# Kernel optimization log

Measured on AMD Instinct MI355X. Metric: run time of the kernel, lower is better.

The kernel has to match this reference:

```python
import jax, jax.numpy as jnp
import numpy as np

N = 4096
INPUT_DIM = 512
KEY_DIM = 64
OUT_DIM = 512
N_HEADS = 8


def _xavier_normal(key, shape, gain):
    # torch xavier_normal_ on [heads, fan_in, fan_out]: fan over last two dims
    fan_in, fan_out = shape[-2], shape[-1]
    std = gain * (2.0 / (fan_in + fan_out)) ** 0.5
    return jax.random.normal(key, shape, dtype=jnp.float32) * std


def setup_inputs() -> dict:
    key = jax.random.key(0)
    kx, ka, kk, kq, kv, ko = jax.random.split(key, 6)
    gain = 2.0 ** 0.5
    node_matrix = jax.random.normal(kx, (N, INPUT_DIM), dtype=jnp.float32)
    adjacency_matrix = jax.random.randint(ka, (N, N), 0, 2).astype(jnp.float32)
    Wks = _xavier_normal(kk, (N_HEADS, INPUT_DIM, KEY_DIM), gain)
    Wqs = _xavier_normal(kq, (N_HEADS, INPUT_DIM, KEY_DIM), gain)
    Wvs = _xavier_normal(kv, (N_HEADS, INPUT_DIM, KEY_DIM), gain)
    Wo = _xavier_normal(ko, (N_HEADS, KEY_DIM, OUT_DIM), gain)
    return {"node_matrix": node_matrix, "adjacency_matrix": adjacency_matrix,
            "Wks": Wks, "Wqs": Wqs, "Wvs": Wvs, "Wo": Wo}


def reference(node_matrix, adjacency_matrix, Wks, Wqs, Wvs, Wo):
    n = adjacency_matrix.shape[0]
    # force self-loops
    adj = jnp.maximum(adjacency_matrix, jnp.eye(n, dtype=adjacency_matrix.dtype))
    # per-head projections: [heads, N, key_dim]
    keys = jnp.einsum('nj,hjk->hnk', node_matrix, Wks)
    queries = jnp.einsum('nj,hjk->hnk', node_matrix, Wqs)
    values = jnp.einsum('nj,hjk->hnk', node_matrix, Wvs)
    key_dim = Wks.shape[-1]
    # [heads, N(query), N(key)] scores, scaled and adjacency-masked
    atts = jnp.einsum('hqk,hmk->hqm', queries, keys) / (key_dim ** 0.5)
    atts = atts - 1e16 * (1.0 - adj)[None, :, :]
    atts = jax.nn.softmax(atts, axis=-1)
    # weighted values, then output projection, summed over heads -> [N, out_dim]
    return jnp.einsum('hqm,hmk,hko->qo', atts, values, Wo)
```

## Files before the change

### kernel.cpp

```cpp
#include <hip/hip_runtime.h>
#include <stdint.h>

typedef unsigned short u16;
typedef __attribute__((ext_vector_type(8))) __bf16 bf16x8;
typedef __attribute__((ext_vector_type(8))) short short8;
typedef __attribute__((ext_vector_type(4))) float f32x4;

#define N_NODES 4096
#define DMODEL  512
#define QKVLD   1536
#define KD      64
#define NH      8
#define NSPLIT  2
#define LOG2E   1.4426950408889634f

static __device__ __forceinline__ u16 f2bf(float f) {
  unsigned u = __builtin_bit_cast(unsigned, f);
  u += 0x7fffu + ((u >> 16) & 1u);
  return (u16)(u >> 16);
}

static __device__ __forceinline__ f32x4 mfma16(short8 a, short8 b, f32x4 c) {
  return __builtin_amdgcn_mfma_f32_16x16x32_bf16(
      __builtin_bit_cast(bf16x8, a), __builtin_bit_cast(bf16x8, b), c, 0, 0, 0);
}

static __device__ __forceinline__ void gload16(const u16* g, u16* l) {
  __builtin_amdgcn_global_load_lds((const __attribute__((address_space(1))) void*)g,
                                   (__attribute__((address_space(3))) void*)l, 16, 0, 0);
}


__global__ void conv_bf16(const float* __restrict__ in, u16* __restrict__ out, int n4) {
  int i = blockIdx.x * blockDim.x + threadIdx.x;
  if (i < n4) {
    float4 v = ((const float4*)in)[i];
    ushort4 o; o.x = f2bf(v.x); o.y = f2bf(v.y); o.z = f2bf(v.z); o.w = f2bf(v.w);
    ((ushort4*)out)[i] = o;
  }
}

__global__ void pack_qkv(const float* __restrict__ Wq, const float* __restrict__ Wk,
                         const float* __restrict__ Wv, u16* __restrict__ Wt) {
  __shared__ float t[64][65];
  int z = blockIdx.z;
  int mat = z >> 3, h = z & 7;
  const float* src = (mat == 0) ? Wq : ((mat == 1) ? Wk : Wv);
  float scale = (mat == 0) ? 0.125f * LOG2E : 1.0f;
  src += (size_t)h * DMODEL * KD;
  u16* dst = Wt + ((size_t)mat * DMODEL + (size_t)h * KD) * DMODEL;
  int r0 = blockIdx.x * 64;
  int tid = threadIdx.x, lc = tid & 63;
#pragma unroll
  for (int i = 0; i < 16; ++i) {
    int row = i * 4 + (tid >> 6);
    t[row][lc] = src[(size_t)(r0 + row) * KD + lc];
  }
  __syncthreads();
#pragma unroll
  for (int i = 0; i < 16; ++i) {
    int row = i * 4 + (tid >> 6);
    dst[(size_t)row * DMODEL + r0 + lc] = f2bf(t[lc][row] * scale);
  }
}

__global__ void pack_wo(const float* __restrict__ Wo, u16* __restrict__ Wot) {
  __shared__ float t[64][65];
  int r0 = blockIdx.x * 64, c0 = blockIdx.y * 64;
  int tid = threadIdx.x, lc = tid & 63;
#pragma unroll
  for (int i = 0; i < 16; ++i) {
    int row = i * 4 + (tid >> 6);
    t[row][lc] = Wo[(size_t)(r0 + row) * 512 + c0 + lc];
  }
  __syncthreads();
#pragma unroll
  for (int i = 0; i < 16; ++i) {
    int row = i * 4 + (tid >> 6);
    Wot[(size_t)(c0 + row) * 512 + r0 + lc] = f2bf(t[lc][row]);
  }
}

__global__ void build_bits(const float* __restrict__ adj, unsigned long long* __restrict__ bits) {
  int gw = (blockIdx.x * blockDim.x + threadIdx.x) >> 6;
  int lane = threadIdx.x & 63;
  int nw = (gridDim.x * blockDim.x) >> 6;
  for (int word = gw; word < N_NODES * 64; word += nw) {
    int q = word >> 6, wc = word & 63;
    int k = wc * 64 + lane;
    float v = adj[(size_t)q * N_NODES + k];
    unsigned long long m = __ballot((v != 0.0f) || (q == k));
    if (lane == 0) bits[word] = m;
  }
}

template <bool OUT_BF16>
__global__ __launch_bounds__(256) void gemm_nt(const u16* __restrict__ A,
                                               const u16* __restrict__ Bt,
                                               void* __restrict__ C, int K,
                                               int lda, int ldb, int ldc,
                                               u16* __restrict__ Vt) {
  __shared__ __align__(16) u16 lA[64 * 64];
  __shared__ __align__(16) u16 lB[64 * 64];
  const int m0 = blockIdx.x * 64, n0 = blockIdx.y * 64;
  const int tid = threadIdx.x;
  const int w = tid >> 6, lane = tid & 63, lm = lane & 15, lg = lane >> 4;
  const int srow = tid >> 2, sc0 = tid & 3;
  f32x4 acc[4] = {};
  for (int k0 = 0; k0 < K; k0 += 64) {
    __syncthreads();
    {
      const short8* ga = (const short8*)(A + (size_t)(m0 + srow) * lda + k0);
      short8* la = (short8*)(lA + srow * 64);
      la[sc0 ^ (srow & 7)] = ga[sc0];
      la[(sc0 + 4) ^ (srow & 7)] = ga[sc0 + 4];
      const short8* gb = (const short8*)(Bt + (size_t)(n0 + srow) * ldb + k0);
      short8* lb = (short8*)(lB + srow * 64);
      lb[sc0 ^ (srow & 7)] = gb[sc0];
      lb[(sc0 + 4) ^ (srow & 7)] = gb[sc0 + 4];
    }
    __syncthreads();
    short8 af0, af1;
    {
      int row = w * 16 + lm;
      af0 = ((short8*)(lA + row * 64))[lg ^ (row & 7)];
      af1 = ((short8*)(lA + row * 64))[(4 + lg) ^ (row & 7)];
    }
#pragma unroll
    for (int nt = 0; nt < 4; ++nt) {
      int row = nt * 16 + lm;
      short8 b0 = ((short8*)(lB + row * 64))[lg ^ (row & 7)];
      short8 b1 = ((short8*)(lB + row * 64))[(4 + lg) ^ (row & 7)];
      acc[nt] = mfma16(af0, b0, acc[nt]);
      acc[nt] = mfma16(af1, b1, acc[nt]);
    }
  }
#pragma unroll
  for (int nt = 0; nt < 4; ++nt) {
    int n = n0 + nt * 16 + lm;
    int mb = m0 + w * 16 + lg * 4;
    if (OUT_BF16) {
      ushort4 o4;
#pragma unroll
      for (int r = 0; r < 4; ++r) ((u16*)&o4)[r] = f2bf(acc[nt][r]);
#pragma unroll
      for (int r = 0; r < 4; ++r) ((u16*)C)[(size_t)(mb + r) * ldc + n] = ((u16*)&o4)[r];
      if (Vt != nullptr && n >= 1024)
        *(ushort4*)(Vt + (size_t)(n - 1024) * N_NODES + mb) = o4;
    } else {
#pragma unroll
      for (int r = 0; r < 4; ++r)
        ((float*)C)[(size_t)(mb + r) * ldc + n] = acc[nt][r];
    }
  }
}

__global__ __launch_bounds__(256, 2) void attn_kernel(const u16* __restrict__ QKV,
                                                      const u16* __restrict__ Vt,
                                                      const unsigned long long* __restrict__ bits,
                                                      float* __restrict__ Op,
                                                      float* __restrict__ lp) {
  __shared__ __align__(16) u16 LDSA[16384 + 4 * 2304];
  const int bid = blockIdx.x;
  const int h = bid & 7, sp = (bid >> 3) & 1, qb = bid >> 4;
  const int tid = threadIdx.x;
  const int w = tid >> 6, lane = tid & 63, lm = lane & 15, lg = lane >> 4;
  const int lg4 = lg * 4;
  const int kb0 = sp * 32;

  const int q0 = qb * 128 + w * 32 + lm;
  const int q1 = q0 + 16;

  const short8 qf00 = *(const short8*)(QKV + (size_t)q0 * QKVLD + h * 64 + lg * 8);
  const short8 qf01 = *(const short8*)(QKV + (size_t)q0 * QKVLD + h * 64 + 32 + lg * 8);
  const short8 qf10 = *(const short8*)(QKV + (size_t)q1 * QKVLD + h * 64 + lg * 8);
  const short8 qf11 = *(const short8*)(QKV + (size_t)q1 * QKVLD + h * 64 + 32 + lg * 8);

  short8 ones;
#pragma unroll
  for (int j = 0; j < 8; ++j) ones[j] = (short)0x3F80;

  const int a0 = lm * 64 + (lg ^ (lm & 7)) * 8;
  const u16* rdA = LDSA + a0;
  const u16* rdB = LDSA + (a0 ^ 32);
  u16* pW0 = LDSA + 16384 + w * 2304 + lm * 72 + lg4;
  u16* pW1 = pW0 + 1152;
  const u16* pR0 = LDSA + 16384 + w * 2304 + lm * 72 + lg * 8;
  const u16* pR1 = pR0 + 1152;

  const int srow = lane >> 3, sc = lane & 7;
  const u16* kP[2]; const u16* vP[2];
#pragma unroll
  for (int i = 0; i < 2; ++i) {
    int row = w * 16 + i * 8 + srow;
    kP[i] = QKV + (size_t)(kb0 * 64 + row) * QKVLD + 512 + h * 64 + (sc ^ (row & 7)) * 8;
    vP[i] = Vt + ((size_t)h * 64 + row) * N_NODES + kb0 * 64 + (sc ^ (row & 7)) * 8;
  }

#define STAGE(buf) do {                                               \
    gload16(kP[0], LDSA + (buf) * 4096 + (w * 2 + 0) * 512);          \
    gload16(kP[1], LDSA + (buf) * 4096 + (w * 2 + 1) * 512);          \
    gload16(vP[0], LDSA + 8192 + (buf) * 4096 + (w * 2 + 0) * 512);   \
    gload16(vP[1], LDSA + 8192 + (buf) * 4096 + (w * 2 + 1) * 512);   \
  } while (0)
#define ADV() do { kP[0] += 64 * QKVLD; kP[1] += 64 * QKVLD; vP[0] += 64; vP[1] += 64; } while (0)

  f32x4 of0[4] = {}, of1[4] = {};
  f32x4 la0 = {}, la1 = {};
  const unsigned long long* bp0 = bits + (size_t)q0 * 64 + kb0;
  const unsigned long long* bp1 = bits + (size_t)q1 * 64 + kb0;

  STAGE(0);
  unsigned long long wb0 = bp0[0], wb1 = bp1[0];

#define SMPACK(sv, wbv, pW, pR, la, paA, paB)                                  \
  do {                                                                         \
    unsigned wlo = (unsigned)((wbv) >> lg4);                                   \
    unsigned whi = ((unsigned)((wbv) >> 32)) >> lg4;                           \
    _Pragma("unroll")                                                          \
    for (int kt = 0; kt < 4; ++kt) {                                           \
      unsigned word = (kt < 2) ? wlo : whi;                                    \
      float pv[4];                                                             \
      _Pragma("unroll")                                                        \
      for (int r = 0; r < 4; ++r) {                                            \
        float e = __builtin_amdgcn_exp2f(sv[kt][r]);                           \
        int mb;                                                                \
        asm("v_bfe_i32 %0, %1, %2, 1" : "=v"(mb)                               \
            : "v"(word), "n"((kt & 1) * 16 + r));                              \
        pv[r] = __builtin_bit_cast(float,                                      \
                   __builtin_bit_cast(unsigned, e) & (unsigned)mb);            \
      }                                                                        \
      unsigned pk0, pk1;                                                       \
      asm("v_cvt_pk_bf16_f32 %0, %1, %2" : "=v"(pk0) : "v"(pv[0]), "v"(pv[1]));\
      asm("v_cvt_pk_bf16_f32 %0, %1, %2" : "=v"(pk1) : "v"(pv[2]), "v"(pv[3]));\
      uint2 pr; pr.x = pk0; pr.y = pk1;                                        \
      *(uint2*)(pW + kt * 16) = pr;                                            \
    }                                                                          \
    paA = *(const short8*)(pR);                                                \
    paB = *(const short8*)(pR + 32);                                           \
    la = mfma16(ones, paA, la);                                                \
    la = mfma16(ones, paB, la);                                                \
  } while (0)

#define BODY(buf, i)                                                           \
  do {                                                                         \
    asm volatile("s_waitcnt vmcnt(0)" ::: "memory");                           \
    __builtin_amdgcn_s_barrier();                                              \
    if ((i) + 1 < 32) { ADV(); STAGE(buf ^ 1); }                               \
    unsigned long long nb0 = ((i) + 1 < 32) ? bp0[(i) + 1] : 0ull;             \
    unsigned long long nb1 = ((i) + 1 < 32) ? bp1[(i) + 1] : 0ull;             \
    f32x4 s0[4], s1[4];                                                        \
    _Pragma("unroll")                                                          \
    for (int kt = 0; kt < 4; ++kt) {                                           \
      short8 k0 = *(const short8*)(rdA + (buf) * 4096 + kt * 1024);            \
      short8 k1 = *(const short8*)(rdB + (buf) * 4096 + kt * 1024);            \
      f32x4 z0 = {0.f, 0.f, 0.f, 0.f}, z1 = {0.f, 0.f, 0.f, 0.f};              \
      z0 = mfma16(k0, qf00, z0); s0[kt] = mfma16(k1, qf01, z0);                \
      z1 = mfma16(k0, qf10, z1); s1[kt] = mfma16(k1, qf11, z1);                \
    }                                                                          \
    short8 pa00, pa01, pa10, pa11;                                             \
    SMPACK(s0, wb0, pW0, pR0, la0, pa00, pa01);                                \
    SMPACK(s1, wb1, pW1, pR1, la1, pa10, pa11);                                \
    _Pragma("unroll")                                                          \
    for (int dt = 0; dt < 4; ++dt) {                                           \
      short8 v0 = *(const short8*)(rdA + 8192 + (buf) * 4096 + dt * 1024);     \
      short8 v1 = *(const short8*)(rdB + 8192 + (buf) * 4096 + dt * 1024);     \
      of0[dt] = mfma16(v0, pa00, of0[dt]);                                     \
      of0[dt] = mfma16(v1, pa01, of0[dt]);                                     \
      of1[dt] = mfma16(v0, pa10, of1[dt]);                                     \
      of1[dt] = mfma16(v1, pa11, of1[dt]);                                     \
    }                                                                          \
    wb0 = nb0; wb1 = nb1;                                                      \
  } while (0)

#pragma unroll 1
  for (int it = 0; it < 16; ++it) {
    BODY(0, it * 2);
    BODY(1, it * 2 + 1);
  }
#undef BODY
#undef SMPACK
#undef STAGE
#undef ADV

  float* Ob = Op + (size_t)sp * N_NODES * DMODEL;
#pragma unroll
  for (int dt = 0; dt < 4; ++dt) {
    *(f32x4*)(Ob + (size_t)q0 * DMODEL + h * 64 + dt * 16 + lg4) = of0[dt];
    *(f32x4*)(Ob + (size_t)q1 * DMODEL + h * 64 + dt * 16 + lg4) = of1[dt];
  }
  if (lg == 0) {
    lp[((size_t)sp * NH + h) * N_NODES + q0] = la0[0];
    lp[((size_t)sp * NH + h) * N_NODES + q1] = la1[0];
  }
}

__global__ __launch_bounds__(256) void combine_kernel(const float* __restrict__ Op,
                                                      const float* __restrict__ lp,
                                                      u16* __restrict__ Oc) {
  int i = blockIdx.x * 256 + threadIdx.x;
  int col = (i * 4) & (DMODEL - 1);
  int q = (i * 4) >> 9;
  int h = col >> 6;
  float4 a = ((const float4*)Op)[i];
  float4 b = ((const float4*)(Op + (size_t)N_NODES * DMODEL))[i];
  float l = lp[(size_t)h * N_NODES + q] + lp[((size_t)NH + h) * N_NODES + q];
  float inv = 1.0f / l;
  ushort4 o;
  o.x = f2bf((a.x + b.x) * inv);
  o.y = f2bf((a.y + b.y) * inv);
  o.z = f2bf((a.z + b.z) * inv);
  o.w = f2bf((a.w + b.w) * inv);
  ((ushort4*)Oc)[i] = o;
}


extern "C" void kernel_launch(void* const* d_in, const int* in_sizes, int n_in,
                              void* d_out, int out_size, void* d_ws, size_t ws_size,
                              hipStream_t stream) {
  const float* X   = (const float*)d_in[0];
  const float* Adj = (const float*)d_in[1];
  const float* Wks = (const float*)d_in[2];
  const float* Wqs = (const float*)d_in[3];
  const float* Wvs = (const float*)d_in[4];
  const float* Wo  = (const float*)d_in[5];

  char* p = (char*)d_ws;
  u16* Xb  = (u16*)p; p += (size_t)N_NODES * DMODEL * 2;
  u16* Wt  = (u16*)p; p += (size_t)3 * DMODEL * DMODEL * 2;
  u16* Wot = (u16*)p; p += (size_t)DMODEL * DMODEL * 2;
  u16* QKV = (u16*)p; p += (size_t)N_NODES * QKVLD * 2;
  u16* Vt  = (u16*)p; p += (size_t)N_NODES * DMODEL * 2;
  u16* Oc  = (u16*)p; p += (size_t)N_NODES * DMODEL * 2;
  unsigned long long* bits = (unsigned long long*)p; p += (size_t)N_NODES * 64 * 8;
  float* Op = (float*)p; p += (size_t)NSPLIT * N_NODES * DMODEL * 4;
  float* lp = (float*)p; p += (size_t)NSPLIT * NH * N_NODES * 4;

  conv_bf16<<<dim3(2048), dim3(256), 0, stream>>>(X, Xb, N_NODES * DMODEL / 4);
  pack_qkv<<<dim3(8, 1, 24), dim3(256), 0, stream>>>(Wqs, Wks, Wvs, Wt);
  pack_wo<<<dim3(8, 8), dim3(256), 0, stream>>>(Wo, Wot);
  build_bits<<<dim3(2048), dim3(256), 0, stream>>>(Adj, bits);

  gemm_nt<true><<<dim3(64, 24), dim3(256), 0, stream>>>(Xb, Wt, QKV, 512, 512, 512, QKVLD, Vt);

  attn_kernel<<<dim3(512), dim3(256), 0, stream>>>(QKV, Vt, bits, Op, lp);
  combine_kernel<<<dim3(N_NODES * DMODEL / 4 / 256), dim3(256), 0, stream>>>(Op, lp, Oc);

  gemm_nt<false><<<dim3(64, 8), dim3(256), 0, stream>>>(Oc, Wot, d_out, 512, 512, 512, 512, nullptr);
}
```

Before: 114.6 us.

## Software-pipeline attention loop across QK, softmax and PV stages

Restructures the attention main loop into a three-stage software pipeline. Each iteration computes QK scores for block i, the masked exp/pack softmax for block i-1 and the PV accumulation for block i-2, with a prologue and epilogue to fill and drain the pipeline. The goal is to let MFMA work from different stages overlap the exp and LDS round-trip latency that previously serialized within each block. To support this, V staging uses four LDS buffers and the per-wave P scratch is shrunk to a single shared region. The cost is more live registers (two sets of score and P fragments), which risks spills under the two-blocks-per-CU launch bound, plus a larger LDS footprint.

```diff
diff --git a/kernel.cpp b/kernel.cpp
--- a/kernel.cpp
+++ b/kernel.cpp
@@ -160,7 +160,7 @@
                                                       const unsigned long long* __restrict__ bits,
                                                       float* __restrict__ Op,
                                                       float* __restrict__ lp) {
-  __shared__ __align__(16) u16 LDSA[16384 + 4 * 2304];
+  __shared__ __align__(16) u16 LDSA[24576 + 4 * 1152];
   const int bid = blockIdx.x;
   const int h = bid & 7, sp = (bid >> 3) & 1, qb = bid >> 4;
   const int tid = threadIdx.x;
@@ -183,10 +183,8 @@
   const int a0 = lm * 64 + (lg ^ (lm & 7)) * 8;
   const u16* rdA = LDSA + a0;
   const u16* rdB = LDSA + (a0 ^ 32);
-  u16* pW0 = LDSA + 16384 + w * 2304 + lm * 72 + lg4;
-  u16* pW1 = pW0 + 1152;
-  const u16* pR0 = LDSA + 16384 + w * 2304 + lm * 72 + lg * 8;
-  const u16* pR1 = pR0 + 1152;
+  u16* pWx = LDSA + 24576 + w * 1152 + lm * 72 + lg4;
+  const u16* pRx = LDSA + 24576 + w * 1152 + lm * 72 + lg * 8;
 
   const int srow = lane >> 3, sc = lane & 7;
   const u16* kP[2]; const u16* vP[2];
@@ -197,11 +195,11 @@
     vP[i] = Vt + ((size_t)h * 64 + row) * N_NODES + kb0 * 64 + (sc ^ (row & 7)) * 8;
   }
 
-#define STAGE(buf) do {                                               \
-    gload16(kP[0], LDSA + (buf) * 4096 + (w * 2 + 0) * 512);          \
-    gload16(kP[1], LDSA + (buf) * 4096 + (w * 2 + 1) * 512);          \
-    gload16(vP[0], LDSA + 8192 + (buf) * 4096 + (w * 2 + 0) * 512);   \
-    gload16(vP[1], LDSA + 8192 + (buf) * 4096 + (w * 2 + 1) * 512);   \
+#define STAGE(kbuf, vbuf) do {                                          \
+    gload16(kP[0], LDSA + (kbuf) * 4096 + (w * 2 + 0) * 512);           \
+    gload16(kP[1], LDSA + (kbuf) * 4096 + (w * 2 + 1) * 512);           \
+    gload16(vP[0], LDSA + 8192 + (vbuf) * 4096 + (w * 2 + 0) * 512);    \
+    gload16(vP[1], LDSA + 8192 + (vbuf) * 4096 + (w * 2 + 1) * 512);    \
   } while (0)
 #define ADV() do { kP[0] += 64 * QKVLD; kP[1] += 64 * QKVLD; vP[0] += 64; vP[1] += 64; } while (0)
 
@@ -210,10 +208,23 @@
   const unsigned long long* bp0 = bits + (size_t)q0 * 64 + kb0;
   const unsigned long long* bp1 = bits + (size_t)q1 * 64 + kb0;
 
-  STAGE(0);
-  unsigned long long wb0 = bp0[0], wb1 = bp1[0];
-
-#define SMPACK(sv, wbv, pW, pR, la, paA, paB)                                  \
+  f32x4 sA0[4], sA1[4], sB0[4], sB1[4];
+  short8 paA00, paA01, paA10, paA11, paB00, paB01, paB10, paB11;
+  unsigned long long wb0, wb1;
+
+#define QKPH(kbuf, S0, S1)                                                     \
+  do {                                                                         \
+    _Pragma("unroll")                                                          \
+    for (int kt = 0; kt < 4; ++kt) {                                           \
+      short8 k0 = *(const short8*)(rdA + (kbuf) * 4096 + kt * 1024);           \
+      short8 k1 = *(const short8*)(rdB + (kbuf) * 4096 + kt * 1024);           \
+      f32x4 z0 = {0.f, 0.f, 0.f, 0.f}, z1 = {0.f, 0.f, 0.f, 0.f};              \
+      z0 = mfma16(k0, qf00, z0); S0[kt] = mfma16(k1, qf01, z0);                \
+      z1 = mfma16(k0, qf10, z1); S1[kt] = mfma16(k1, qf11, z1);                \
+    }                                                                          \
+  } while (0)
+
+#define SMPK(sv, wbv, la, paA, paB)                                            \
   do {                                                                         \
     unsigned wlo = (unsigned)((wbv) >> lg4);                                   \
     unsigned whi = ((unsigned)((wbv) >> 32)) >> lg4;                           \
@@ -234,52 +245,77 @@
       asm("v_cvt_pk_bf16_f32 %0, %1, %2" : "=v"(pk0) : "v"(pv[0]), "v"(pv[1]));\
       asm("v_cvt_pk_bf16_f32 %0, %1, %2" : "=v"(pk1) : "v"(pv[2]), "v"(pv[3]));\
       uint2 pr; pr.x = pk0; pr.y = pk1;                                        \
-      *(uint2*)(pW + kt * 16) = pr;                                            \
+      *(uint2*)(pWx + kt * 16) = pr;                                           \
     }                                                                          \
-    paA = *(const short8*)(pR);                                                \
-    paB = *(const short8*)(pR + 32);                                           \
+    paA = *(const short8*)(pRx);                                               \
+    paB = *(const short8*)(pRx + 32);                                          \
     la = mfma16(ones, paA, la);                                                \
     la = mfma16(ones, paB, la);                                                \
   } while (0)
 
-#define BODY(buf, i)                                                           \
+#define PVPH(vbuf, p00, p01, p10, p11)                                         \
+  do {                                                                         \
+    _Pragma("unroll")                                                          \
+    for (int dt = 0; dt < 4; ++dt) {                                           \
+      short8 v0 = *(const short8*)(rdA + 8192 + (vbuf) * 4096 + dt * 1024);    \
+      short8 v1 = *(const short8*)(rdB + 8192 + (vbuf) * 4096 + dt * 1024);    \
+      of0[dt] = mfma16(v0, p00, of0[dt]);                                      \
+      of0[dt] = mfma16(v1, p01, of0[dt]);                                      \
+      of1[dt] = mfma16(v0, p10, of1[dt]);                                      \
+      of1[dt] = mfma16(v1, p11, of1[dt]);                                      \
+    }                                                                          \
+  } while (0)
+
+#define ITERM(IDX, KBQ, SQ0, SQ1, DO_STAGE, KST, VST, DO_SM, SS0, SS1,         \
+              PW00, PW01, PW10, PW11, DO_PV, VPV, PR00, PR01, PR10, PR11)      \
   do {                                                                         \
     asm volatile("s_waitcnt vmcnt(0)" ::: "memory");                           \
     __builtin_amdgcn_s_barrier();                                              \
-    if ((i) + 1 < 32) { ADV(); STAGE(buf ^ 1); }                               \
-    unsigned long long nb0 = ((i) + 1 < 32) ? bp0[(i) + 1] : 0ull;             \
-    unsigned long long nb1 = ((i) + 1 < 32) ? bp1[(i) + 1] : 0ull;             \
-    f32x4 s0[4], s1[4];                                                        \
-    _Pragma("unroll")                                                          \
-    for (int kt = 0; kt < 4; ++kt) {                                           \
-      short8 k0 = *(const short8*)(rdA + (buf) * 4096 + kt * 1024);            \
-      short8 k1 = *(const short8*)(rdB + (buf) * 4096 + kt * 1024);            \
-      f32x4 z0 = {0.f, 0.f, 0.f, 0.f}, z1 = {0.f, 0.f, 0.f, 0.f};              \
-      z0 = mfma16(k0, qf00, z0); s0[kt] = mfma16(k1, qf01, z0);                \
-      z1 = mfma16(k0, qf10, z1); s1[kt] = mfma16(k1, qf11, z1);                \
+    if (DO_STAGE) { ADV(); STAGE(KST, VST); }                                  \
+    unsigned long long nb0 = bp0[IDX], nb1 = bp1[IDX];                         \
+    QKPH(KBQ, SQ0, SQ1);                                                       \
+    if (DO_SM) {                                                               \
+      SMPK(SS0, wb0, la0, PW00, PW01);                                         \
+      SMPK(SS1, wb1, la1, PW10, PW11);                                         \
     }                                                                          \
-    short8 pa00, pa01, pa10, pa11;                                             \
-    SMPACK(s0, wb0, pW0, pR0, la0, pa00, pa01);                                \
-    SMPACK(s1, wb1, pW1, pR1, la1, pa10, pa11);                                \
-    _Pragma("unroll")                                                          \
-    for (int dt = 0; dt < 4; ++dt) {                                           \
-      short8 v0 = *(const short8*)(rdA + 8192 + (buf) * 4096 + dt * 1024);     \
-      short8 v1 = *(const short8*)(rdB + 8192 + (buf) * 4096 + dt * 1024);     \
-      of0[dt] = mfma16(v0, pa00, of0[dt]);                                     \
-      of0[dt] = mfma16(v1, pa01, of0[dt]);                                     \
-      of1[dt] = mfma16(v0, pa10, of1[dt]);                                     \
-      of1[dt] = mfma16(v1, pa11, of1[dt]);                                     \
-    }                                                                          \
+    if (DO_PV) { PVPH(VPV, PR00, PR01, PR10, PR11); }                          \
     wb0 = nb0; wb1 = nb1;                                                      \
   } while (0)
 
+  STAGE(0, 0);
+
+  ITERM(0, 0, sA0, sA1, true, 1, 1, false, sB0, sB1,
+        paA00, paA01, paA10, paA11, false, 0, paA00, paA01, paA10, paA11);
+  ITERM(1, 1, sB0, sB1, true, 0, 2, true, sA0, sA1,
+        paA00, paA01, paA10, paA11, false, 0, paB00, paB01, paB10, paB11);
+
 #pragma unroll 1
-  for (int it = 0; it < 16; ++it) {
-    BODY(0, it * 2);
-    BODY(1, it * 2 + 1);
-  }
-#undef BODY
-#undef SMPACK
+  for (int t = 0; t < 7; ++t) {
+    const int b = 2 + 4 * t;
+    ITERM(b + 0, 0, sA0, sA1, true, 1, 3, true, sB0, sB1,
+          paB00, paB01, paB10, paB11, true, 0, paA00, paA01, paA10, paA11);
+    ITERM(b + 1, 1, sB0, sB1, true, 0, 0, true, sA0, sA1,
+          paA00, paA01, paA10, paA11, true, 1, paB00, paB01, paB10, paB11);
+    ITERM(b + 2, 0, sA0, sA1, true, 1, 1, true, sB0, sB1,
+          paB00, paB01, paB10, paB11, true, 2, paA00, paA01, paA10, paA11);
+    ITERM(b + 3, 1, sB0, sB1, true, 0, 2, true, sA0, sA1,
+          paA00, paA01, paA10, paA11, true, 3, paB00, paB01, paB10, paB11);
+  }
+
+  ITERM(30, 0, sA0, sA1, true, 1, 3, true, sB0, sB1,
+        paB00, paB01, paB10, paB11, true, 0, paA00, paA01, paA10, paA11);
+  ITERM(31, 1, sB0, sB1, false, 0, 0, true, sA0, sA1,
+        paA00, paA01, paA10, paA11, true, 1, paB00, paB01, paB10, paB11);
+
+  SMPK(sB0, wb0, la0, paB00, paB01);
+  SMPK(sB1, wb1, la1, paB10, paB11);
+  PVPH(2, paA00, paA01, paA10, paA11);
+  PVPH(3, paB00, paB01, paB10, paB11);
+
+#undef ITERM
+#undef PVPH
+#undef SMPK
+#undef QKPH
 #undef STAGE
 #undef ADV
 
```

Result: no change. 113.3 us (-1.1%).

## Double queries per attention block and split keys four ways

Applied to the files above, without the earlier changes.

Each attention wave now processes four 16-row query subtiles (256 queries per block) instead of two, so every K/V tile staged in LDS is reused across twice as many queries. The key range is split into four partitions instead of two, keeping the block count unchanged. The combine kernel now sums four partial outputs and normalizers. The trade-off is more accumulator and Q-fragment registers per thread, plus doubled partial-output traffic in the combine step.

```diff
diff --git a/kernel.cpp b/kernel.cpp
--- a/kernel.cpp
+++ b/kernel.cpp
@@ -11,7 +11,7 @@
 #define QKVLD   1536
 #define KD      64
 #define NH      8
-#define NSPLIT  2
+#define NSPLIT  4
 #define LOG2E   1.4426950408889634f
 
 static __device__ __forceinline__ u16 f2bf(float f) {
@@ -162,19 +162,20 @@
                                                       float* __restrict__ lp) {
   __shared__ __align__(16) u16 LDSA[16384 + 4 * 2304];
   const int bid = blockIdx.x;
-  const int h = bid & 7, sp = (bid >> 3) & 1, qb = bid >> 4;
+  const int h = bid & 7, sp = (bid >> 3) & 3, qb = bid >> 5;
   const int tid = threadIdx.x;
   const int w = tid >> 6, lane = tid & 63, lm = lane & 15, lg = lane >> 4;
   const int lg4 = lg * 4;
-  const int kb0 = sp * 32;
-
-  const int q0 = qb * 128 + w * 32 + lm;
-  const int q1 = q0 + 16;
-
-  const short8 qf00 = *(const short8*)(QKV + (size_t)q0 * QKVLD + h * 64 + lg * 8);
-  const short8 qf01 = *(const short8*)(QKV + (size_t)q0 * QKVLD + h * 64 + 32 + lg * 8);
-  const short8 qf10 = *(const short8*)(QKV + (size_t)q1 * QKVLD + h * 64 + lg * 8);
-  const short8 qf11 = *(const short8*)(QKV + (size_t)q1 * QKVLD + h * 64 + 32 + lg * 8);
+  const int kb0 = sp * 16;
+  const int q0 = qb * 256 + w * 64 + lm;
+
+  short8 qf[4][2];
+#pragma unroll
+  for (int s = 0; s < 4; ++s) {
+    const u16* qp = QKV + (size_t)(q0 + 16 * s) * QKVLD + h * 64;
+    qf[s][0] = *(const short8*)(qp + lg * 8);
+    qf[s][1] = *(const short8*)(qp + 32 + lg * 8);
+  }
 
   short8 ones;
 #pragma unroll
@@ -205,93 +206,101 @@
   } while (0)
 #define ADV() do { kP[0] += 64 * QKVLD; kP[1] += 64 * QKVLD; vP[0] += 64; vP[1] += 64; } while (0)
 
-  f32x4 of0[4] = {}, of1[4] = {};
-  f32x4 la0 = {}, la1 = {};
-  const unsigned long long* bp0 = bits + (size_t)q0 * 64 + kb0;
-  const unsigned long long* bp1 = bits + (size_t)q1 * 64 + kb0;
+  f32x4 of[4][4] = {};
+  f32x4 la[4] = {};
+  const unsigned long long* bp[4];
+#pragma unroll
+  for (int s = 0; s < 4; ++s) bp[s] = bits + (size_t)(q0 + 16 * s) * 64 + kb0;
 
   STAGE(0);
-  unsigned long long wb0 = bp0[0], wb1 = bp1[0];
-
-#define SMPACK(sv, wbv, pW, pR, la, paA, paB)                                  \
-  do {                                                                         \
-    unsigned wlo = (unsigned)((wbv) >> lg4);                                   \
-    unsigned whi = ((unsigned)((wbv) >> 32)) >> lg4;                           \
-    _Pragma("unroll")                                                          \
-    for (int kt = 0; kt < 4; ++kt) {                                           \
-      unsigned word = (kt < 2) ? wlo : whi;                                    \
-      float pv[4];                                                             \
-      _Pragma("unroll")                                                        \
-      for (int r = 0; r < 4; ++r) {                                            \
-        float e = __builtin_amdgcn_exp2f(sv[kt][r]);                           \
-        int mb;                                                                \
-        asm("v_bfe_i32 %0, %1, %2, 1" : "=v"(mb)                               \
-            : "v"(word), "n"((kt & 1) * 16 + r));                              \
-        pv[r] = __builtin_bit_cast(float,                                      \
-                   __builtin_bit_cast(unsigned, e) & (unsigned)mb);            \
-      }                                                                        \
-      unsigned pk0, pk1;                                                       \
-      asm("v_cvt_pk_bf16_f32 %0, %1, %2" : "=v"(pk0) : "v"(pv[0]), "v"(pv[1]));\
-      asm("v_cvt_pk_bf16_f32 %0, %1, %2" : "=v"(pk1) : "v"(pv[2]), "v"(pv[3]));\
-      uint2 pr; pr.x = pk0; pr.y = pk1;                                        \
-      *(uint2*)(pW + kt * 16) = pr;                                            \
-    }                                                                          \
-    paA = *(const short8*)(pR);                                                \
-    paB = *(const short8*)(pR + 32);                                           \
-    la = mfma16(ones, paA, la);                                                \
-    la = mfma16(ones, paB, la);                                                \
-  } while (0)
+  unsigned long long wb[4];
+#pragma unroll
+  for (int s = 0; s < 4; ++s) wb[s] = bp[s][0];
 
 #define BODY(buf, i)                                                           \
   do {                                                                         \
     asm volatile("s_waitcnt vmcnt(0)" ::: "memory");                           \
     __builtin_amdgcn_s_barrier();                                              \
-    if ((i) + 1 < 32) { ADV(); STAGE(buf ^ 1); }                               \
-    unsigned long long nb0 = ((i) + 1 < 32) ? bp0[(i) + 1] : 0ull;             \
-    unsigned long long nb1 = ((i) + 1 < 32) ? bp1[(i) + 1] : 0ull;             \
-    f32x4 s0[4], s1[4];                                                        \
+    if ((i) + 1 < 16) { ADV(); STAGE(buf ^ 1); }                               \
+    unsigned long long nb[4];                                                  \
+    _Pragma("unroll")                                                          \
+    for (int s = 0; s < 4; ++s) nb[s] = ((i) + 1 < 16) ? bp[s][(i) + 1] : 0ull;\
+                            \
+    short8 kf[4][2];                                                           \
     _Pragma("unroll")                                                          \
     for (int kt = 0; kt < 4; ++kt) {                                           \
-      short8 k0 = *(const short8*)(rdA + (buf) * 4096 + kt * 1024);            \
-      short8 k1 = *(const short8*)(rdB + (buf) * 4096 + kt * 1024);            \
-      f32x4 z0 = {0.f, 0.f, 0.f, 0.f}, z1 = {0.f, 0.f, 0.f, 0.f};              \
-      z0 = mfma16(k0, qf00, z0); s0[kt] = mfma16(k1, qf01, z0);                \
-      z1 = mfma16(k0, qf10, z1); s1[kt] = mfma16(k1, qf11, z1);                \
+      kf[kt][0] = *(const short8*)(rdA + (buf) * 4096 + kt * 1024);            \
+      kf[kt][1] = *(const short8*)(rdB + (buf) * 4096 + kt * 1024);            \
     }                                                                          \
-    short8 pa00, pa01, pa10, pa11;                                             \
-    SMPACK(s0, wb0, pW0, pR0, la0, pa00, pa01);                                \
-    SMPACK(s1, wb1, pW1, pR1, la1, pa10, pa11);                                \
+    short8 pa[4][2];                                                           \
+    _Pragma("unroll")                                                          \
+    for (int s = 0; s < 4; ++s) {                                              \
+      f32x4 ss[4];                                                             \
+      _Pragma("unroll")                                                        \
+      for (int kt = 0; kt < 4; ++kt) {                                         \
+        f32x4 z = {0.f, 0.f, 0.f, 0.f};                                        \
+        z = mfma16(kf[kt][0], qf[s][0], z);                                    \
+        ss[kt] = mfma16(kf[kt][1], qf[s][1], z);                               \
+      }                                                                        \
+      unsigned wlo = (unsigned)(wb[s] >> lg4);                                 \
+      unsigned whi = ((unsigned)(wb[s] >> 32)) >> lg4;                         \
+      u16* pWs = (s & 1) ? pW1 : pW0;                                          \
+      const u16* pRs = (s & 1) ? pR1 : pR0;                                    \
+      _Pragma("unroll")                                                        \
+      for (int kt = 0; kt < 4; ++kt) {                                         \
+        unsigned word = (kt < 2) ? wlo : whi;                                  \
+        float pv[4];                                                           \
+        _Pragma("unroll")                                                      \
+        for (int r = 0; r < 4; ++r) {                                          \
+          float e = __builtin_amdgcn_exp2f(ss[kt][r]);                         \
+          int mb;                                                              \
+          asm("v_bfe_i32 %0, %1, %2, 1" : "=v"(mb)                             \
+              : "v"(word), "n"((kt & 1) * 16 + r));                            \
+          pv[r] = __builtin_bit_cast(float,                                    \
+                     __builtin_bit_cast(unsigned, e) & (unsigned)mb);          \
+        }                                                                      \
+        unsigned pk0, pk1;                                                     \
+        asm("v_cvt_pk_bf16_f32 %0, %1, %2" : "=v"(pk0) : "v"(pv[0]), "v"(pv[1]));\
+        asm("v_cvt_pk_bf16_f32 %0, %1, %2" : "=v"(pk1) : "v"(pv[2]), "v"(pv[3]));\
+        uint2 pr; pr.x = pk0; pr.y = pk1;                                      \
+        *(uint2*)(pWs + kt * 16) = pr;                                         \
+      }                                                                        \
+      pa[s][0] = *(const short8*)(pRs);                                        \
+      pa[s][1] = *(const short8*)(pRs + 32);                                   \
+      la[s] = mfma16(ones, pa[s][0], la[s]);                                   \
+      la[s] = mfma16(ones, pa[s][1], la[s]);                                   \
+    }                                                                          \
+                       \
     _Pragma("unroll")                                                          \
     for (int dt = 0; dt < 4; ++dt) {                                           \
       short8 v0 = *(const short8*)(rdA + 8192 + (buf) * 4096 + dt * 1024);     \
       short8 v1 = *(const short8*)(rdB + 8192 + (buf) * 4096 + dt * 1024);     \
-      of0[dt] = mfma16(v0, pa00, of0[dt]);                                     \
-      of0[dt] = mfma16(v1, pa01, of0[dt]);                                     \
-      of1[dt] = mfma16(v0, pa10, of1[dt]);                                     \
-      of1[dt] = mfma16(v1, pa11, of1[dt]);                                     \
+      _Pragma("unroll")                                                        \
+      for (int s = 0; s < 4; ++s) {                                            \
+        of[s][dt] = mfma16(v0, pa[s][0], of[s][dt]);                           \
+        of[s][dt] = mfma16(v1, pa[s][1], of[s][dt]);                           \
+      }                                                                        \
     }                                                                          \
-    wb0 = nb0; wb1 = nb1;                                                      \
+    _Pragma("unroll")                                                          \
+    for (int s = 0; s < 4; ++s) wb[s] = nb[s];                                 \
   } while (0)
 
 #pragma unroll 1
-  for (int it = 0; it < 16; ++it) {
+  for (int it = 0; it < 8; ++it) {
     BODY(0, it * 2);
     BODY(1, it * 2 + 1);
   }
 #undef BODY
-#undef SMPACK
 #undef STAGE
 #undef ADV
 
   float* Ob = Op + (size_t)sp * N_NODES * DMODEL;
 #pragma unroll
-  for (int dt = 0; dt < 4; ++dt) {
-    *(f32x4*)(Ob + (size_t)q0 * DMODEL + h * 64 + dt * 16 + lg4) = of0[dt];
-    *(f32x4*)(Ob + (size_t)q1 * DMODEL + h * 64 + dt * 16 + lg4) = of1[dt];
-  }
-  if (lg == 0) {
-    lp[((size_t)sp * NH + h) * N_NODES + q0] = la0[0];
-    lp[((size_t)sp * NH + h) * N_NODES + q1] = la1[0];
+  for (int s = 0; s < 4; ++s) {
+#pragma unroll
+    for (int dt = 0; dt < 4; ++dt)
+      *(f32x4*)(Ob + (size_t)(q0 + 16 * s) * DMODEL + h * 64 + dt * 16 + lg4) = of[s][dt];
+    if (lg == 0) lp[((size_t)sp * NH + h) * N_NODES + q0 + 16 * s] = la[s][0];
   }
 }
 
@@ -302,15 +311,20 @@
   int col = (i * 4) & (DMODEL - 1);
   int q = (i * 4) >> 9;
   int h = col >> 6;
-  float4 a = ((const float4*)Op)[i];
-  float4 b = ((const float4*)(Op + (size_t)N_NODES * DMODEL))[i];
-  float l = lp[(size_t)h * N_NODES + q] + lp[((size_t)NH + h) * N_NODES + q];
+  float4 acc = {0.f, 0.f, 0.f, 0.f};
+  float l = 0.f;
+#pragma unroll
+  for (int sp = 0; sp < NSPLIT; ++sp) {
+    float4 a = ((const float4*)(Op + (size_t)sp * N_NODES * DMODEL))[i];
+    acc.x += a.x; acc.y += a.y; acc.z += a.z; acc.w += a.w;
+    l += lp[((size_t)sp * NH + h) * N_NODES + q];
+  }
   float inv = 1.0f / l;
   ushort4 o;
-  o.x = f2bf((a.x + b.x) * inv);
-  o.y = f2bf((a.y + b.y) * inv);
-  o.z = f2bf((a.z + b.z) * inv);
-  o.w = f2bf((a.w + b.w) * inv);
+  o.x = f2bf(acc.x * inv);
+  o.y = f2bf(acc.y * inv);
+  o.z = f2bf(acc.z * inv);
+  o.w = f2bf(acc.w * inv);
   ((ushort4*)Oc)[i] = o;
 }
 
```

Result: slower. 117.8 us (+2.9%).

## Use 512-thread attention blocks with four-way key split

Applied to the files above, without the earlier changes.

The attention kernel now runs 8 waves per block covering 256 queries, so each staged K/V tile in LDS is shared by twice as many query rows. The key range is split four ways instead of two, which keeps the grid at 512 blocks and halves the loop length per block. The combine kernel now sums four partial outputs and denominators, adding extra global traffic for the partial buffers. Launch bounds change to 512 threads with 4 blocks per CU, which may tighten register limits.

```diff
diff --git a/kernel.cpp b/kernel.cpp
--- a/kernel.cpp
+++ b/kernel.cpp
@@ -11,7 +11,7 @@
 #define QKVLD   1536
 #define KD      64
 #define NH      8
-#define NSPLIT  2
+#define NSPLIT  4
 #define LOG2E   1.4426950408889634f
 
 static __device__ __forceinline__ u16 f2bf(float f) {
@@ -155,20 +155,20 @@
   }
 }
 
-__global__ __launch_bounds__(256, 2) void attn_kernel(const u16* __restrict__ QKV,
+__global__ __launch_bounds__(512, 4) void attn_kernel(const u16* __restrict__ QKV,
                                                       const u16* __restrict__ Vt,
                                                       const unsigned long long* __restrict__ bits,
                                                       float* __restrict__ Op,
                                                       float* __restrict__ lp) {
-  __shared__ __align__(16) u16 LDSA[16384 + 4 * 2304];
+  __shared__ __align__(16) u16 LDSA[16384 + 8 * 2304];
   const int bid = blockIdx.x;
-  const int h = bid & 7, sp = (bid >> 3) & 1, qb = bid >> 4;
+  const int h = bid & 7, sp = (bid >> 3) & 3, qb = bid >> 5;
   const int tid = threadIdx.x;
   const int w = tid >> 6, lane = tid & 63, lm = lane & 15, lg = lane >> 4;
   const int lg4 = lg * 4;
-  const int kb0 = sp * 32;
-
-  const int q0 = qb * 128 + w * 32 + lm;
+  const int kb0 = sp * 16;
+
+  const int q0 = qb * 256 + w * 32 + lm;
   const int q1 = q0 + 16;
 
   const short8 qf00 = *(const short8*)(QKV + (size_t)q0 * QKVLD + h * 64 + lg * 8);
@@ -189,21 +189,15 @@
   const u16* pR1 = pR0 + 1152;
 
   const int srow = lane >> 3, sc = lane & 7;
-  const u16* kP[2]; const u16* vP[2];
-#pragma unroll
-  for (int i = 0; i < 2; ++i) {
-    int row = w * 16 + i * 8 + srow;
-    kP[i] = QKV + (size_t)(kb0 * 64 + row) * QKVLD + 512 + h * 64 + (sc ^ (row & 7)) * 8;
-    vP[i] = Vt + ((size_t)h * 64 + row) * N_NODES + kb0 * 64 + (sc ^ (row & 7)) * 8;
-  }
-
-#define STAGE(buf) do {                                               \
-    gload16(kP[0], LDSA + (buf) * 4096 + (w * 2 + 0) * 512);          \
-    gload16(kP[1], LDSA + (buf) * 4096 + (w * 2 + 1) * 512);          \
-    gload16(vP[0], LDSA + 8192 + (buf) * 4096 + (w * 2 + 0) * 512);   \
-    gload16(vP[1], LDSA + 8192 + (buf) * 4096 + (w * 2 + 1) * 512);   \
+  const int grow = w * 8 + srow;
+  const u16* kP = QKV + (size_t)(kb0 * 64 + grow) * QKVLD + 512 + h * 64 + (sc ^ srow) * 8;
+  const u16* vP = Vt + ((size_t)h * 64 + grow) * N_NODES + kb0 * 64 + (sc ^ srow) * 8;
+
+#define STAGE(buf) do {                                   \
+    gload16(kP, LDSA + (buf) * 4096 + w * 512);           \
+    gload16(vP, LDSA + 8192 + (buf) * 4096 + w * 512);    \
   } while (0)
-#define ADV() do { kP[0] += 64 * QKVLD; kP[1] += 64 * QKVLD; vP[0] += 64; vP[1] += 64; } while (0)
+#define ADV() do { kP += 64 * QKVLD; vP += 64; } while (0)
 
   f32x4 of0[4] = {}, of1[4] = {};
   f32x4 la0 = {}, la1 = {};
@@ -246,9 +240,9 @@
   do {                                                                         \
     asm volatile("s_waitcnt vmcnt(0)" ::: "memory");                           \
     __builtin_amdgcn_s_barrier();                                              \
-    if ((i) + 1 < 32) { ADV(); STAGE(buf ^ 1); }                               \
-    unsigned long long nb0 = ((i) + 1 < 32) ? bp0[(i) + 1] : 0ull;             \
-    unsigned long long nb1 = ((i) + 1 < 32) ? bp1[(i) + 1] : 0ull;             \
+    if ((i) + 1 < 16) { ADV(); STAGE(buf ^ 1); }                               \
+    unsigned long long nb0 = ((i) + 1 < 16) ? bp0[(i) + 1] : 0ull;             \
+    unsigned long long nb1 = ((i) + 1 < 16) ? bp1[(i) + 1] : 0ull;             \
     f32x4 s0[4], s1[4];                                                        \
     _Pragma("unroll")                                                          \
     for (int kt = 0; kt < 4; ++kt) {                                           \
@@ -274,7 +268,7 @@
   } while (0)
 
 #pragma unroll 1
-  for (int it = 0; it < 16; ++it) {
+  for (int it = 0; it < 8; ++it) {
     BODY(0, it * 2);
     BODY(1, it * 2 + 1);
   }
@@ -302,15 +296,20 @@
   int col = (i * 4) & (DMODEL - 1);
   int q = (i * 4) >> 9;
   int h = col >> 6;
-  float4 a = ((const float4*)Op)[i];
-  float4 b = ((const float4*)(Op + (size_t)N_NODES * DMODEL))[i];
-  float l = lp[(size_t)h * N_NODES + q] + lp[((size_t)NH + h) * N_NODES + q];
+  float4 acc = {0.f, 0.f, 0.f, 0.f};
+  float l = 0.f;
+#pragma unroll
+  for (int sp = 0; sp < NSPLIT; ++sp) {
+    float4 a = ((const float4*)(Op + (size_t)sp * N_NODES * DMODEL))[i];
+    acc.x += a.x; acc.y += a.y; acc.z += a.z; acc.w += a.w;
+    l += lp[((size_t)sp * NH + h) * N_NODES + q];
+  }
   float inv = 1.0f / l;
   ushort4 o;
-  o.x = f2bf((a.x + b.x) * inv);
-  o.y = f2bf((a.y + b.y) * inv);
-  o.z = f2bf((a.z + b.z) * inv);
-  o.w = f2bf((a.w + b.w) * inv);
+  o.x = f2bf(acc.x * inv);
+  o.y = f2bf(acc.y * inv);
+  o.z = f2bf(acc.z * inv);
+  o.w = f2bf(acc.w * inv);
   ((ushort4*)Oc)[i] = o;
 }
 
@@ -343,7 +342,7 @@
 
   gemm_nt<true><<<dim3(64, 24), dim3(256), 0, stream>>>(Xb, Wt, QKV, 512, 512, 512, QKVLD, Vt);
 
-  attn_kernel<<<dim3(512), dim3(256), 0, stream>>>(QKV, Vt, bits, Op, lp);
+  attn_kernel<<<dim3(512), dim3(512), 0, stream>>>(QKV, Vt, bits, Op, lp);
   combine_kernel<<<dim3(N_NODES * DMODEL / 4 / 256), dim3(256), 0, stream>>>(Op, lp, Oc);
 
   gemm_nt<false><<<dim3(64, 8), dim3(256), 0, stream>>>(Oc, Wot, d_out, 512, 512, 512, 512, nullptr);
```

New measurement: 114.9 us. Within noise of the previous version (+0.3%).
